# Kernel optimization log

Hardware: AMD Instinct MI355X
Metric: run time of the kernel (lower is better)

Reference implementation:

```python
import jax, jax.numpy as jnp
import numpy as np

H = 512      # hidden_size (hardcoded in __init__)
WD = 1024    # word_dim (hardcoded)
V = 4096     # len(i2w)+4
B, S, T = 256, 80, 28


def setup_inputs() -> dict:
    key = jax.random.key(0)
    ks = jax.random.split(key, 14)

    def gl(k, shape, fan_in):
        return (jax.random.normal(k, shape, jnp.float32) / np.sqrt(fan_in)).astype(jnp.float32)

    return {
        "encoder_last_hidden_state": jax.random.normal(ks[0], (1, B, H), jnp.float32),
        "encoder_output": jax.random.normal(ks[1], (B, S, H), jnp.float32),
        "targets": jax.random.randint(ks[2], (B, T), 0, V, dtype=jnp.int32),
        # embedding table
        "embedding": gl(ks[3], (V, WD), WD),
        # attention MLP (4 stacked linears, no activations, per the source)
        "W1": gl(ks[4], (2 * H, H), 2 * H), "b1": jnp.zeros((H,), jnp.float32),
        "W2": gl(ks[5], (H, H), H), "b2": jnp.zeros((H,), jnp.float32),
        "W3": gl(ks[6], (H, H), H), "b3": jnp.zeros((H,), jnp.float32),
        "W4": gl(ks[7], (H, H), H), "b4": jnp.zeros((H,), jnp.float32),
        "Ww": gl(ks[8], (H, 1), H),
        # GRU (input = hidden_size + word_dim = 1536), PyTorch gate order r,z,n
        "W_ih": gl(ks[9], (3 * H, H + WD), H + WD), "b_ih": jnp.zeros((3 * H,), jnp.float32),
        "W_hh": gl(ks[10], (3 * H, H), H), "b_hh": jnp.zeros((3 * H,), jnp.float32),
        # output projection
        "Wo": gl(ks[11], (H, V), H), "bo": jnp.zeros((V,), jnp.float32),
    }


def reference(encoder_last_hidden_state, encoder_output, targets, embedding,
              W1, b1, W2, b2, W3, b3, W4, b4, Ww,
              W_ih, b_ih, W_hh, b_hh, Wo, bo):
    n_steps = targets.shape[1] - 1  # seq_len - 1 decode steps

    def attention(h, enc):
        # h: (B,H) decoder hidden; enc: (B,S,H)
        hs = jnp.broadcast_to(h[:, None, :], enc.shape)
        m = jnp.concatenate([enc, hs], axis=-1)          # (B,S,2H)
        x = m @ W1 + b1
        x = x @ W2 + b2
        x = x @ W3 + b3
        x = x @ W4 + b4
        attw = jax.nn.softmax((x @ Ww)[..., 0], axis=1)  # (B,S)
        return jnp.einsum('bs,bsh->bh', attw, enc)       # context (B,H)

    def gru_cell(x, h):
        gi = x @ W_ih.T + b_ih
        gh = h @ W_hh.T + b_hh
        ir, iz, inn = jnp.split(gi, 3, axis=-1)
        hr, hz, hn = jnp.split(gh, 3, axis=-1)
        r = jax.nn.sigmoid(ir + hr)
        z = jax.nn.sigmoid(iz + hz)
        n = jnp.tanh(inn + r * hn)
        return (1.0 - z) * n + z * h

    h0 = encoder_last_hidden_state[0]                    # (B,H)
    w0 = jnp.ones((encoder_output.shape[0],), jnp.int32) # <BOS> = 1

    def step(carry, _):
        h, w = carry
        emb = embedding[w]                               # (B,WD)
        ctx = attention(h, encoder_output)               # (B,H)
        x = jnp.concatenate([emb, ctx], axis=-1)         # (B,WD+H)
        hn = gru_cell(x, h)
        logits = hn @ Wo + bo                            # (B,V)
        wn = jnp.argmax(logits, axis=-1).astype(jnp.int32)
        return (hn, wn), logits

    _, logits_seq = jax.lax.scan(step, (h0, w0), None, length=n_steps)
    seq_logProb = jnp.swapaxes(logits_seq, 0, 1)         # (B, T-1, V)
    seq_predictions = jnp.argmax(seq_logProb, axis=-1)
    return seq_logProb, seq_predictions
```

## Files before the change

kernel.cpp:

```cpp
#include <hip/hip_runtime.h>

#define B_ 256
#define S_ 80
#define H_ 512
#define V_ 4096
#define NSTEP 27

typedef unsigned short u16;
typedef __attribute__((ext_vector_type(8))) short short8v;
typedef __attribute__((ext_vector_type(4))) float f32x4;
typedef __attribute__((ext_vector_type(4))) unsigned short ushort4v;

#define MFMA_(a,b,c) __builtin_amdgcn_mfma_f32_16x16x32_bf16(a,b,c,0,0,0)
#define MFMA3(acc, ah, al, bh, bl) do{ acc = MFMA_(ah,bh,acc); acc = MFMA_(ah,bl,acc); acc = MFMA_(al,bh,acc);}while(0)

__device__ __forceinline__ unsigned fkey(float v){
    unsigned u = __float_as_uint(v);
    return (u & 0x80000000u) ? ~u : (u | 0x80000000u);
}
__device__ __forceinline__ u16 bf16_rne(float f){
    unsigned u = __float_as_uint(f);
    return (u16)((u + 0x7FFFu + ((u >> 16) & 1u)) >> 16);
}
__device__ __forceinline__ void split_f4(float4 v, ushort4v& hi, ushort4v& lo){
    float arr[4] = {v.x, v.y, v.z, v.w};
    ushort4v h, l;
#pragma unroll
    for (int i = 0; i < 4; ++i){
        u16 hb = bf16_rne(arr[i]);
        h[i] = hb;
        l[i] = bf16_rne(arr[i] - __uint_as_float(((unsigned)hb) << 16));
    }
    hi = h; lo = l;
}

__global__ __launch_bounds__(64) void matvec512(const float* __restrict__ W,
                                                const float* __restrict__ v,
                                                float* __restrict__ out){
    int row = blockIdx.x, lane = threadIdx.x;
    const float* wr = W + row * 512;
    float s = 0.f;
#pragma unroll
    for (int i = 0; i < 8; ++i) s += wr[lane + 64*i] * v[lane + 64*i];
#pragma unroll
    for (int off = 32; off; off >>= 1) s += __shfl_xor(s, off);
    if (lane == 0) out[row] = s;
}

__global__ __launch_bounds__(256) void prep_all(
    const float* __restrict__ Whh, const float* __restrict__ Wo,
    const float* __restrict__ emb, const float* __restrict__ Wih,
    const float* __restrict__ elhs,
    u16* __restrict__ WhhHi, u16* __restrict__ WhhLo,
    u16* __restrict__ WoThi, u16* __restrict__ WoTlo,
    u16* __restrict__ EmbHi, u16* __restrict__ EmbLo,
    u16* __restrict__ WihLHi, u16* __restrict__ WihLLo,
    u16* __restrict__ Sh, u16* __restrict__ Sl,
    unsigned* __restrict__ zp, int nz)
{
    __shared__ float T[64][65];
    int b = blockIdx.x, tid = threadIdx.x;
    if (b < 768){
        int idx = (b*256 + tid)*4;
        float4 v = *(const float4*)&Whh[idx];
        ushort4v h,l; split_f4(v,h,l);
        *(ushort4v*)&WhhHi[idx]=h; *(ushort4v*)&WhhLo[idx]=l;
    } else if (b < 1280){
        int lb = b - 768;
        int k0 = (lb & 7)*64, n0 = (lb >> 3)*64;
#pragma unroll
        for (int i = 0; i < 16; ++i){
            int idx = tid + i*256;
            int kk = idx >> 6, nn = idx & 63;
            T[kk][nn] = Wo[(size_t)(k0+kk)*4096 + n0+nn];
        }
        __syncthreads();
#pragma unroll
        for (int i = 0; i < 16; ++i){
            int idx = tid + i*256;
            int nn = idx >> 6, kk = idx & 63;
            float v = T[kk][nn];
            u16 hi = bf16_rne(v);
            u16 lo = bf16_rne(v - __uint_as_float(((unsigned)hi) << 16));
            size_t o = (size_t)(n0+nn)*512 + k0+kk;
            WoThi[o] = hi; WoTlo[o] = lo;
        }
    } else if (b < 5376){
        int idx = ((b-1280)*256 + tid)*4;
        float4 v = *(const float4*)&emb[idx];
        ushort4v h,l; split_f4(v,h,l);
        *(ushort4v*)&EmbHi[idx]=h; *(ushort4v*)&EmbLo[idx]=l;
    } else if (b < 6912){
        int id = ((b-5376)*256 + tid)*4;
        int r = id >> 10, c = id & 1023;
        float4 v = *(const float4*)&Wih[(size_t)r*1536 + c];
        ushort4v h,l; split_f4(v,h,l);
        *(ushort4v*)&WihLHi[id]=h; *(ushort4v*)&WihLLo[id]=l;
    } else if (b < 7040){
        int idx = ((b-6912)*256 + tid)*4;
        float4 v = *(const float4*)&elhs[idx];
        ushort4v h,l; split_f4(v,h,l);
        *(ushort4v*)&Sh[idx]=h; *(ushort4v*)&Sl[idx]=l;
    } else {
        int i = ((b-7040)*256 + tid)*4;
        if (i < nz){ zp[i]=0u; zp[i+1]=0u; zp[i+2]=0u; zp[i+3]=0u; }
    }
}

__global__ __launch_bounds__(512) void attn_ctx(const float* __restrict__ enc,
                                                const float* __restrict__ weff,
                                                float* __restrict__ ctx){
    __shared__ float att[S_];
    int b = blockIdx.x, tid = threadIdx.x;
    int wv = tid >> 6, lane = tid & 63;
    float w8[8];
#pragma unroll
    for (int i = 0; i < 8; ++i) w8[i] = weff[lane + 64*i];
    const float* eb = enc + (size_t)b * (S_*H_);
    for (int s = wv; s < S_; s += 8){
        const float* e = eb + s*512;
        float acc = 0.f;
#pragma unroll
        for (int i = 0; i < 8; ++i) acc += e[lane + 64*i] * w8[i];
#pragma unroll
        for (int off = 32; off; off >>= 1) acc += __shfl_xor(acc, off);
        if (lane == 0) att[s] = acc;
    }
    __syncthreads();
    if (tid == 0){
        float mx = att[0];
        for (int s = 1; s < S_; ++s) mx = fmaxf(mx, att[s]);
        float sum = 0.f;
        for (int s = 0; s < S_; ++s){ float e = expf(att[s] - mx); att[s] = e; sum += e; }
        float inv = 1.f / sum;
        for (int s = 0; s < S_; ++s) att[s] *= inv;
    }
    __syncthreads();
    float a = 0.f;
    for (int s = 0; s < S_; ++s) a += att[s] * eb[s*512 + tid];
    ctx[b*512 + tid] = a;
}

__device__ __forceinline__ void step_mm_body(char* smem, int m0, int nt, int n_logits,
    const u16* __restrict__ Ahg, const u16* __restrict__ Alg,
    const u16* __restrict__ WoHi, const u16* __restrict__ WoLo,
    const u16* __restrict__ WhhHi, const u16* __restrict__ WhhLo,
    const float* __restrict__ bo,
    float* __restrict__ logits, unsigned long long* __restrict__ Pcur,
    float* __restrict__ gh_out)
{
    u16 (*Ah)[2048] = (u16(*)[2048])(smem);
    u16 (*Al)[2048] = (u16(*)[2048])(smem + 8192);
    u16 (*Bh)[2048] = (u16(*)[2048])(smem + 16384);
    u16 (*Bl)[2048] = (u16(*)[2048])(smem + 24576);
    bool isL = nt < n_logits;
    int nbase = (isL ? nt : nt - n_logits) * 64;
    const u16* Bhg = isL ? WoHi : WhhHi;
    const u16* Blg = isL ? WoLo : WhhLo;
    int tid = threadIdx.x, lane = tid & 63, wid = tid >> 6;
    int wy = wid & 1, wx = wid >> 1;
    int l15 = lane & 15, rg = lane >> 4, lk = rg * 8;
    int sr = tid >> 2, sk8 = (tid & 3) * 8;

    const u16* gAh = Ahg + (size_t)(m0 + sr)*512 + sk8;
    const u16* gAl = Alg + (size_t)(m0 + sr)*512 + sk8;
    const u16* gBh = Bhg + (size_t)(nbase + sr)*512 + sk8;
    const u16* gBl = Blg + (size_t)(nbase + sr)*512 + sk8;

    *(short8v*)&Ah[0][tid*8] = *(const short8v*)gAh;
    *(short8v*)&Al[0][tid*8] = *(const short8v*)gAl;
    *(short8v*)&Bh[0][tid*8] = *(const short8v*)gBh;
    *(short8v*)&Bl[0][tid*8] = *(const short8v*)gBl;
    short8v r1a = *(const short8v*)(gAh + 32), r1b = *(const short8v*)(gAl + 32);
    short8v r1c = *(const short8v*)(gBh + 32), r1d = *(const short8v*)(gBl + 32);
    short8v r2a = *(const short8v*)(gAh + 64), r2b = *(const short8v*)(gAl + 64);
    short8v r2c = *(const short8v*)(gBh + 64), r2d = *(const short8v*)(gBl + 64);
    __syncthreads();

    f32x4 acc[2][2] = {};
    int p = 0;
    for (int k0 = 0; k0 < 512; k0 += 32){
        if (k0 + 32 < 512){
            *(short8v*)&Ah[p^1][tid*8] = r1a;
            *(short8v*)&Al[p^1][tid*8] = r1b;
            *(short8v*)&Bh[p^1][tid*8] = r1c;
            *(short8v*)&Bl[p^1][tid*8] = r1d;
            r1a = r2a; r1b = r2b; r1c = r2c; r1d = r2d;
            if (k0 + 96 < 512){
                r2a = *(const short8v*)(gAh + k0 + 96);
                r2b = *(const short8v*)(gAl + k0 + 96);
                r2c = *(const short8v*)(gBh + k0 + 96);
                r2d = *(const short8v*)(gBl + k0 + 96);
            }
        }
        short8v afh0 = *(const short8v*)&Ah[p][(wy*32 +  0 + l15)*32 + lk];
        short8v afh1 = *(const short8v*)&Ah[p][(wy*32 + 16 + l15)*32 + lk];
        short8v afl0 = *(const short8v*)&Al[p][(wy*32 +  0 + l15)*32 + lk];
        short8v afl1 = *(const short8v*)&Al[p][(wy*32 + 16 + l15)*32 + lk];
        short8v bfh0 = *(const short8v*)&Bh[p][(wx*32 +  0 + l15)*32 + lk];
        short8v bfh1 = *(const short8v*)&Bh[p][(wx*32 + 16 + l15)*32 + lk];
        short8v bfl0 = *(const short8v*)&Bl[p][(wx*32 +  0 + l15)*32 + lk];
        short8v bfl1 = *(const short8v*)&Bl[p][(wx*32 + 16 + l15)*32 + lk];
        MFMA3(acc[0][0], afh0, afl0, bfh0, bfl0);
        MFMA3(acc[0][1], afh0, afl0, bfh1, bfl1);
        MFMA3(acc[1][0], afh1, afl1, bfh0, bfl0);
        MFMA3(acc[1][1], afh1, afl1, bfh1, bfl1);
        __syncthreads();
        p ^= 1;
    }

    int col0 = nbase + wx*32 + l15;
    if (isL){
        float bo0 = bo[col0], bo1 = bo[col0 + 16];
#pragma unroll
        for (int mf = 0; mf < 2; ++mf){
#pragma unroll
            for (int r = 0; r < 4; ++r){
                int row = m0 + wy*32 + mf*16 + rg*4 + r;
                float v0 = acc[mf][0][r] + bo0;
                float v1 = acc[mf][1][r] + bo1;
                float* crow = logits + (size_t)row * (NSTEP * (size_t)V_);
                crow[col0]      = v0;
                crow[col0 + 16] = v1;
                unsigned long long k0_ = ((unsigned long long)fkey(v0) << 32) | (unsigned)(4095 - col0);
                unsigned long long k1_ = ((unsigned long long)fkey(v1) << 32) | (unsigned)(4095 - (col0+16));
                unsigned long long best = k0_ > k1_ ? k0_ : k1_;
#pragma unroll
                for (int off = 1; off < 16; off <<= 1){
                    unsigned long long o = __shfl_xor(best, off);
                    if (o > best) best = o;
                }
                if (l15 == 0) atomicMax(&Pcur[row], best);
            }
        }
    } else {
#pragma unroll
        for (int mf = 0; mf < 2; ++mf)
#pragma unroll
            for (int r = 0; r < 4; ++r){
                int row = m0 + wy*32 + mf*16 + rg*4 + r;
                gh_out[(size_t)row*1536 + col0]      = acc[mf][0][r];
                gh_out[(size_t)row*1536 + col0 + 16] = acc[mf][1][r];
            }
    }
}

__global__ __launch_bounds__(256) void front3(
    const u16* __restrict__ EmbHi, const u16* __restrict__ EmbLo,
    const u16* __restrict__ WihLHi, const u16* __restrict__ WihLLo,
    float* __restrict__ Eproj,
    const float* __restrict__ ctx, const float* __restrict__ WihR,
    const float* __restrict__ bih, float* __restrict__ gictx,
    const u16* __restrict__ Sh0, const u16* __restrict__ Sl0,
    const u16* __restrict__ WhhHi, const u16* __restrict__ WhhLo,
    float* __restrict__ gh0)
{
    __shared__ __align__(16) char smem[32768];
    int b = blockIdx.x, tid = threadIdx.x;
    if (b < 384){
        int work = (b & 7) * 48 + (b >> 3);
        int bm = work / 12, bn = work % 12;
        int n0 = bn * 128, m0 = bm * 128;
        int lane = tid & 63, wid = tid >> 6;
        int wy = wid & 1, wx = wid >> 1;
        int l15 = lane & 15, rg = lane >> 4, lk = rg * 8;
        u16* Ah = (u16*)smem;
        u16* Al = (u16*)(smem + 8192);
        u16* Bh = (u16*)(smem + 16384);
        u16* Bl = (u16*)(smem + 24576);
        const u16* gA[2][2]; const u16* gB[2][2];
#pragma unroll
        for (int j = 0; j < 2; ++j){
            int s = tid + j*256;
            int row = s >> 2, k8 = (s & 3)*8;
            gA[0][j] = EmbHi + (size_t)(m0+row)*1024 + k8;
            gA[1][j] = EmbLo + (size_t)(m0+row)*1024 + k8;
            gB[0][j] = WihLHi + (size_t)(n0+row)*1024 + k8;
            gB[1][j] = WihLLo + (size_t)(n0+row)*1024 + k8;
        }
        short8v rA[2][2], rB[2][2];
#pragma unroll
        for (int h = 0; h < 2; ++h)
#pragma unroll
            for (int j = 0; j < 2; ++j){
                rA[h][j] = *(const short8v*)gA[h][j];
                rB[h][j] = *(const short8v*)gB[h][j];
            }
        f32x4 acc[4][4] = {};
        for (int k0 = 0; k0 < 1024; k0 += 32){
            __syncthreads();
#pragma unroll
            for (int j = 0; j < 2; ++j){
                int s8 = (tid + j*256)*8;
                *(short8v*)&Ah[s8] = rA[0][j];
                *(short8v*)&Al[s8] = rA[1][j];
                *(short8v*)&Bh[s8] = rB[0][j];
                *(short8v*)&Bl[s8] = rB[1][j];
            }
            __syncthreads();
            if (k0 + 32 < 1024){
#pragma unroll
                for (int h = 0; h < 2; ++h)
#pragma unroll
                    for (int j = 0; j < 2; ++j){
                        rA[h][j] = *(const short8v*)(gA[h][j] + k0 + 32);
                        rB[h][j] = *(const short8v*)(gB[h][j] + k0 + 32);
                    }
            }
            short8v afh[4], afl[4];
#pragma unroll
            for (int mf = 0; mf < 4; ++mf){
                afh[mf] = *(const short8v*)&Ah[(wy*64 + mf*16 + l15)*32 + lk];
                afl[mf] = *(const short8v*)&Al[(wy*64 + mf*16 + l15)*32 + lk];
            }
#pragma unroll
            for (int nf = 0; nf < 4; ++nf){
                short8v bfh = *(const short8v*)&Bh[(wx*64 + nf*16 + l15)*32 + lk];
                short8v bfl = *(const short8v*)&Bl[(wx*64 + nf*16 + l15)*32 + lk];
#pragma unroll
                for (int mf = 0; mf < 4; ++mf)
                    MFMA3(acc[mf][nf], afh[mf], afl[mf], bfh, bfl);
            }
        }
        int col0 = n0 + wx*64 + l15;
#pragma unroll
        for (int mf = 0; mf < 4; ++mf)
#pragma unroll
            for (int r = 0; r < 4; ++r){
                int row = m0 + wy*64 + mf*16 + rg*4 + r;
#pragma unroll
                for (int nf = 0; nf < 4; ++nf)
                    Eproj[(size_t)row*1536 + col0 + nf*16] = acc[mf][nf][r];
            }
    } else if (b < 576){
        int lb = b - 384;
        int m0 = (lb & 7) * 32, n0 = (lb >> 3) * 64;
        float (*As)[36] = (float(*)[36])smem;
        float (*Bs)[68] = (float(*)[68])(smem + 2304);
        int lk = tid & 15, lr = tid >> 4;
        int tx = tid & 15, ty = tid >> 4;
        float c[2][4] = {};
        for (int k0 = 0; k0 < 512; k0 += 16){
#pragma unroll
            for (int i = 0; i < 2; ++i)
                As[lk][lr*2 + i] = ctx[(size_t)(m0 + lr*2 + i)*512 + k0 + lk];
#pragma unroll
            for (int i = 0; i < 4; ++i)
                Bs[lk][lr*4 + i] = WihR[(size_t)(n0 + lr*4 + i)*1536 + k0 + lk];
            __syncthreads();
#pragma unroll
            for (int k = 0; k < 16; ++k){
                float b4[4];
                *(float4*)b4 = *(const float4*)&Bs[k][tx*4];
#pragma unroll
                for (int i = 0; i < 2; ++i){
                    float a = As[k][ty*2 + i];
#pragma unroll
                    for (int j = 0; j < 4; ++j) c[i][j] += a * b4[j];
                }
            }
            __syncthreads();
        }
#pragma unroll
        for (int j = 0; j < 4; ++j){
            float bb = bih[n0 + tx*4 + j];
#pragma unroll
            for (int i = 0; i < 2; ++i)
                gictx[(size_t)(m0 + ty*2 + i)*1536 + n0 + tx*4 + j] = c[i][j] + bb;
        }
    } else {
        int lb = b - 576;
        step_mm_body(smem, (lb & 3)*64, lb >> 2, 0,
                     Sh0, Sl0, nullptr, nullptr, WhhHi, WhhLo,
                     nullptr, nullptr, nullptr, gh0);
    }
}

__global__ __launch_bounds__(128) void gru_pointwise(
    const float* __restrict__ gh, const float* __restrict__ Eproj,
    const float* __restrict__ gictx, const float* __restrict__ bhh,
    const float* __restrict__ hprev, float* __restrict__ hnext,
    u16* __restrict__ Sh, u16* __restrict__ Sl,
    const unsigned long long* __restrict__ Pprev,
    float* __restrict__ preds, int t)
{
    int tid = threadIdx.x;
    int row = blockIdx.x;
    int jj = tid * 4;
    int w = 1;
    if (t > 0){
        w = 4095 - (int)(Pprev[row] & 0xFFFFFFFFull);
        if (w < 0) w = 0; if (w > 4095) w = 4095;
        if (tid == 0) preds[row*NSTEP + (t-1)] = (float)w;
    }
    const float* gr = gh + (size_t)row * 1536;
    const float* ep = Eproj + (size_t)w * 1536;
    const float* gc = gictx + (size_t)row * 1536;
    float4 g0 = *(const float4*)&gr[jj];
    float4 g1 = *(const float4*)&gr[512 + jj];
    float4 g2 = *(const float4*)&gr[1024 + jj];
    float4 e0 = *(const float4*)&ep[jj];
    float4 e1 = *(const float4*)&ep[512 + jj];
    float4 e2 = *(const float4*)&ep[1024 + jj];
    float4 c0 = *(const float4*)&gc[jj];
    float4 c1 = *(const float4*)&gc[512 + jj];
    float4 c2 = *(const float4*)&gc[1024 + jj];
    float4 b0 = *(const float4*)&bhh[jj];
    float4 b1 = *(const float4*)&bhh[512 + jj];
    float4 b2 = *(const float4*)&bhh[1024 + jj];
    float4 ho = *(const float4*)&hprev[(size_t)row*512 + jj];
    const float* G0 = (const float*)&g0; const float* G1 = (const float*)&g1;
    const float* G2 = (const float*)&g2;
    const float* E0 = (const float*)&e0; const float* E1 = (const float*)&e1;
    const float* E2 = (const float*)&e2;
    const float* C0 = (const float*)&c0; const float* C1 = (const float*)&c1;
    const float* C2 = (const float*)&c2;
    const float* B0 = (const float*)&b0; const float* B1 = (const float*)&b1;
    const float* B2 = (const float*)&b2;
    const float* HO = (const float*)&ho;
    float4 res;
    float* R = (float*)&res;
#pragma unroll
    for (int i = 0; i < 4; ++i){
        float gir = E0[i] + C0[i] + G0[i] + B0[i];
        float giz = E1[i] + C1[i] + G1[i] + B1[i];
        float gin = E2[i] + C2[i];
        float rr = 1.f / (1.f + expf(-gir));
        float zz = 1.f / (1.f + expf(-giz));
        float nn = tanhf(gin + rr * (G2[i] + B2[i]));
        R[i] = (1.f - zz)*nn + zz*HO[i];
    }
    size_t o = (size_t)row*512 + jj;
    *(float4*)&hnext[o] = res;
    ushort4v h4, l4; split_f4(res, h4, l4);
    *(ushort4v*)&Sh[o] = h4;
    *(ushort4v*)&Sl[o] = l4;
}

__global__ __launch_bounds__(256) void step_mm(
    const u16* __restrict__ Ahg, const u16* __restrict__ Alg,
    const u16* __restrict__ WoHi, const u16* __restrict__ WoLo,
    const u16* __restrict__ WhhHi, const u16* __restrict__ WhhLo,
    const float* __restrict__ bo,
    float* __restrict__ logits, unsigned long long* __restrict__ Pcur,
    float* __restrict__ gh_out, int n_logits)
{
    __shared__ __align__(16) char smem[24576];
    u16 (*Ah)[1024] = (u16(*)[1024])(smem);
    u16 (*Al)[1024] = (u16(*)[1024])(smem + 4096);
    u16 (*Bh)[2048] = (u16(*)[2048])(smem + 8192);
    u16 (*Bl)[2048] = (u16(*)[2048])(smem + 16384);
    int bid = blockIdx.x;
    int work = (bid & 7) * 88 + (bid >> 3);
    int m0 = (work & 7) * 32;
    int nt = work >> 3;
    bool isL = nt < n_logits;
    int nbase = (isL ? nt : nt - n_logits) * 64;
    const u16* Bhg = isL ? WoHi : WhhHi;
    const u16* Blg = isL ? WoLo : WhhLo;
    int tid = threadIdx.x, lane = tid & 63, wid = tid >> 6;
    int wy = wid & 1, wx = wid >> 1;
    int l15 = lane & 15, rg = lane >> 4, lk = rg * 8;

    int ahalf = tid >> 7, ai = tid & 127;
    int ar = ai >> 2, ak8 = (ai & 3) * 8;
    const u16* gA = (ahalf ? Alg : Ahg) + (size_t)(m0 + ar)*512 + ak8;
    u16 (*Adst)[1024] = ahalf ? Al : Ah;
    int br = tid >> 2, bk8 = (tid & 3) * 8;
    const u16* gBh = Bhg + (size_t)(nbase + br)*512 + bk8;
    const u16* gBl = Blg + (size_t)(nbase + br)*512 + bk8;

    *(short8v*)&Adst[0][ai*8] = *(const short8v*)gA;
    *(short8v*)&Bh[0][tid*8] = *(const short8v*)gBh;
    *(short8v*)&Bl[0][tid*8] = *(const short8v*)gBl;
    short8v a1 = *(const short8v*)(gA + 32),  a2 = *(const short8v*)(gA + 64);
    short8v h1 = *(const short8v*)(gBh + 32), h2 = *(const short8v*)(gBh + 64);
    short8v l1 = *(const short8v*)(gBl + 32), l2 = *(const short8v*)(gBl + 64);
    __syncthreads();

    f32x4 acc[2] = {};
    int p = 0;
    for (int k0 = 0; k0 < 512; k0 += 32){
        if (k0 + 32 < 512){
            *(short8v*)&Adst[p^1][ai*8] = a1;
            *(short8v*)&Bh[p^1][tid*8] = h1;
            *(short8v*)&Bl[p^1][tid*8] = l1;
            a1 = a2; h1 = h2; l1 = l2;
            if (k0 + 96 < 512){
                a2 = *(const short8v*)(gA + k0 + 96);
                h2 = *(const short8v*)(gBh + k0 + 96);
                l2 = *(const short8v*)(gBl + k0 + 96);
            }
        }
        short8v afh = *(const short8v*)&Ah[p][(wy*16 + l15)*32 + lk];
        short8v afl = *(const short8v*)&Al[p][(wy*16 + l15)*32 + lk];
        short8v bfh0 = *(const short8v*)&Bh[p][(wx*32 +  0 + l15)*32 + lk];
        short8v bfh1 = *(const short8v*)&Bh[p][(wx*32 + 16 + l15)*32 + lk];
        short8v bfl0 = *(const short8v*)&Bl[p][(wx*32 +  0 + l15)*32 + lk];
        short8v bfl1 = *(const short8v*)&Bl[p][(wx*32 + 16 + l15)*32 + lk];
        MFMA3(acc[0], afh, afl, bfh0, bfl0);
        MFMA3(acc[1], afh, afl, bfh1, bfl1);
        __syncthreads();
        p ^= 1;
    }

    int col0 = nbase + wx*32 + l15;
    if (isL){
        float bo0 = bo[col0], bo1 = bo[col0 + 16];
#pragma unroll
        for (int r = 0; r < 4; ++r){
            int row = m0 + wy*16 + rg*4 + r;
            float v0 = acc[0][r] + bo0;
            float v1 = acc[1][r] + bo1;
            float* crow = logits + (size_t)row * (NSTEP * (size_t)V_);
            crow[col0]      = v0;
            crow[col0 + 16] = v1;
            unsigned long long k0_ = ((unsigned long long)fkey(v0) << 32) | (unsigned)(4095 - col0);
            unsigned long long k1_ = ((unsigned long long)fkey(v1) << 32) | (unsigned)(4095 - (col0+16));
            unsigned long long best = k0_ > k1_ ? k0_ : k1_;
#pragma unroll
            for (int off = 1; off < 16; off <<= 1){
                unsigned long long o = __shfl_xor(best, off);
                if (o > best) best = o;
            }
            if (l15 == 0) atomicMax(&Pcur[row], best);
        }
    } else {
#pragma unroll
        for (int r = 0; r < 4; ++r){
            int row = m0 + wy*16 + rg*4 + r;
            gh_out[(size_t)row*1536 + col0]      = acc[0][r];
            gh_out[(size_t)row*1536 + col0 + 16] = acc[1][r];
        }
    }
}

__global__ __launch_bounds__(256) void final_pred(const unsigned long long* __restrict__ P,
                                                  float* __restrict__ preds){
    int b = threadIdx.x;
    int w = 4095 - (int)(P[b] & 0xFFFFFFFFull);
    if (w < 0) w = 0; if (w > 4095) w = 4095;
    preds[b*NSTEP + (NSTEP-1)] = (float)w;
}

extern "C" void kernel_launch(void* const* d_in, const int* in_sizes, int n_in,
                              void* d_out, int out_size, void* d_ws, size_t ws_size,
                              hipStream_t stream){
    const float* elhs = (const float*)d_in[0];
    const float* enc  = (const float*)d_in[1];
    const float* emb  = (const float*)d_in[3];
    const float* W1   = (const float*)d_in[4];
    const float* W2   = (const float*)d_in[6];
    const float* W3   = (const float*)d_in[8];
    const float* W4   = (const float*)d_in[10];
    const float* Ww   = (const float*)d_in[12];
    const float* Wih  = (const float*)d_in[13];
    const float* bih  = (const float*)d_in[14];
    const float* Whh  = (const float*)d_in[15];
    const float* bhh  = (const float*)d_in[16];
    const float* Wo   = (const float*)d_in[17];
    const float* bo   = (const float*)d_in[18];

    float* out = (float*)d_out;
    float* preds = out + (size_t)B_ * NSTEP * V_;

    float* ws = (float*)d_ws;
    float* Eproj  = ws;  ws += (size_t)V_ * 1536;
    float* gictx  = ws;  ws += (size_t)B_ * 1536;
    float* ctx    = ws;  ws += B_ * H_;
    float* t1     = ws;  ws += 512;
    float* t2     = ws;  ws += 512;
    float* weff   = ws;  ws += 512;
    float* Hf     = ws;  ws += 2 * B_ * H_;
    float* ghbuf  = ws;  ws += B_ * 1536;
    u16* WoT_hi = (u16*)ws;  ws += (size_t)V_ * 512 / 2;
    u16* WoT_lo = (u16*)ws;  ws += (size_t)V_ * 512 / 2;
    u16* WhhHi  = (u16*)ws;  ws += 1536 * 512 / 2;
    u16* WhhLo  = (u16*)ws;  ws += 1536 * 512 / 2;
    u16* Sh     = (u16*)ws;  ws += B_ * H_ / 2;
    u16* Sl     = (u16*)ws;  ws += B_ * H_ / 2;
    unsigned long long* P = (unsigned long long*)ws;

    u16* EmbHi  = (u16*)d_out;
    u16* EmbLo  = EmbHi + (size_t)V_*1024;
    u16* WihLHi = EmbLo + (size_t)V_*1024;
    u16* WihLLo = WihLHi + (size_t)1536*1024;

    prep_all<<<7054, 256, 0, stream>>>(Whh, Wo, emb, Wih, elhs,
                                       WhhHi, WhhLo, WoT_hi, WoT_lo,
                                       EmbHi, EmbLo, WihLHi, WihLLo,
                                       Sh, Sl, (unsigned*)P, NSTEP*256*2);
    matvec512<<<512, 64, 0, stream>>>(W4, Ww, t1);
    matvec512<<<512, 64, 0, stream>>>(W3, t1, t2);
    matvec512<<<512, 64, 0, stream>>>(W2, t2, t1);
    matvec512<<<512, 64, 0, stream>>>(W1, t1, weff);
    attn_ctx<<<B_, 512, 0, stream>>>(enc, weff, ctx);
    front3<<<672, 256, 0, stream>>>(EmbHi, EmbLo, WihLHi, WihLLo, Eproj,
                                    ctx, Wih + 1024, bih, gictx,
                                    Sh, Sl, WhhHi, WhhLo, ghbuf);

    for (int t = 0; t < NSTEP; ++t){
        const float* hr = (t == 0) ? elhs : (Hf + (size_t)((t-1) & 1) * (B_*H_));
        float*       hw = Hf + (size_t)(t & 1) * (B_*H_);
        const unsigned long long* Pprev = P + (size_t)(t > 0 ? t-1 : 0) * 256;
        gru_pointwise<<<256, 128, 0, stream>>>(ghbuf, Eproj, gictx, bhh, hr, hw,
                                               Sh, Sl, Pprev, preds, t);
        step_mm<<<704, 256, 0, stream>>>(Sh, Sl, WoT_hi, WoT_lo, WhhHi, WhhLo, bo,
                                         out + (size_t)t * V_, P + (size_t)t*256, ghbuf, 64);
    }
    final_pred<<<1, 256, 0, stream>>>(P + (size_t)(NSTEP-1)*256, preds);
}
```

Baseline: 693.0 us.

## Double-buffer LDS in front3 GEMM and fold first matvec into prep kernel

The embedding-projection GEMM in front3 now uses two LDS buffers with a two-stage register prefetch, so each k-step needs one barrier instead of two and global loads run further ahead. Shared memory per block doubles to 64KB, which may lower occupancy. Separately, the W4·Ww matvec is merged into prep_all as extra blocks, removing one kernel launch from the serial chain.

```diff
diff --git a/kernel.cpp b/kernel.cpp
--- a/kernel.cpp
+++ b/kernel.cpp
@@ -51,11 +51,13 @@
     const float* __restrict__ Whh, const float* __restrict__ Wo,
     const float* __restrict__ emb, const float* __restrict__ Wih,
     const float* __restrict__ elhs,
+    const float* __restrict__ W4, const float* __restrict__ Ww,
     u16* __restrict__ WhhHi, u16* __restrict__ WhhLo,
     u16* __restrict__ WoThi, u16* __restrict__ WoTlo,
     u16* __restrict__ EmbHi, u16* __restrict__ EmbLo,
     u16* __restrict__ WihLHi, u16* __restrict__ WihLLo,
     u16* __restrict__ Sh, u16* __restrict__ Sl,
+    float* __restrict__ t1out,
     unsigned* __restrict__ zp, int nz)
 {
     __shared__ float T[64][65];
@@ -101,9 +103,19 @@
         float4 v = *(const float4*)&elhs[idx];
         ushort4v h,l; split_f4(v,h,l);
         *(ushort4v*)&Sh[idx]=h; *(ushort4v*)&Sl[idx]=l;
-    } else {
+    } else if (b < 7054){
         int i = ((b-7040)*256 + tid)*4;
         if (i < nz){ zp[i]=0u; zp[i+1]=0u; zp[i+2]=0u; zp[i+3]=0u; }
+    } else {
+        int lane = tid & 63, wv = tid >> 6;
+        int row = (b - 7054)*4 + wv;
+        const float* wr = W4 + (size_t)row * 512;
+        float s = 0.f;
+#pragma unroll
+        for (int i = 0; i < 8; ++i) s += wr[lane + 64*i] * Ww[lane + 64*i];
+#pragma unroll
+        for (int off = 32; off; off >>= 1) s += __shfl_xor(s, off);
+        if (lane == 0) t1out[row] = s;
     }
 }
 
@@ -255,7 +267,7 @@
     const u16* __restrict__ WhhHi, const u16* __restrict__ WhhLo,
     float* __restrict__ gh0)
 {
-    __shared__ __align__(16) char smem[32768];
+    __shared__ __align__(16) char smem[65536];
     int b = blockIdx.x, tid = threadIdx.x;
     if (b < 384){
         int work = (b & 7) * 48 + (b >> 3);
@@ -264,63 +276,86 @@
         int lane = tid & 63, wid = tid >> 6;
         int wy = wid & 1, wx = wid >> 1;
         int l15 = lane & 15, rg = lane >> 4, lk = rg * 8;
-        u16* Ah = (u16*)smem;
-        u16* Al = (u16*)(smem + 8192);
-        u16* Bh = (u16*)(smem + 16384);
-        u16* Bl = (u16*)(smem + 24576);
+        u16* AhB = (u16*)smem;
+        u16* AlB = (u16*)(smem + 16384);
+        u16* BhB = (u16*)(smem + 32768);
+        u16* BlB = (u16*)(smem + 49152);
         const u16* gA[2][2]; const u16* gB[2][2];
+        int s8i[2];
 #pragma unroll
         for (int j = 0; j < 2; ++j){
             int s = tid + j*256;
             int row = s >> 2, k8 = (s & 3)*8;
+            s8i[j] = s * 8;
             gA[0][j] = EmbHi + (size_t)(m0+row)*1024 + k8;
             gA[1][j] = EmbLo + (size_t)(m0+row)*1024 + k8;
             gB[0][j] = WihLHi + (size_t)(n0+row)*1024 + k8;
             gB[1][j] = WihLLo + (size_t)(n0+row)*1024 + k8;
         }
-        short8v rA[2][2], rB[2][2];
+#pragma unroll
+        for (int j = 0; j < 2; ++j){
+            *(short8v*)&AhB[s8i[j]] = *(const short8v*)gA[0][j];
+            *(short8v*)&AlB[s8i[j]] = *(const short8v*)gA[1][j];
+            *(short8v*)&BhB[s8i[j]] = *(const short8v*)gB[0][j];
+            *(short8v*)&BlB[s8i[j]] = *(const short8v*)gB[1][j];
+        }
+        short8v r1A[2][2], r1B[2][2], r2A[2][2], r2B[2][2];
 #pragma unroll
         for (int h = 0; h < 2; ++h)
 #pragma unroll
             for (int j = 0; j < 2; ++j){
-                rA[h][j] = *(const short8v*)gA[h][j];
-                rB[h][j] = *(const short8v*)gB[h][j];
-            }
+                r1A[h][j] = *(const short8v*)(gA[h][j] + 32);
+                r1B[h][j] = *(const short8v*)(gB[h][j] + 32);
+                r2A[h][j] = *(const short8v*)(gA[h][j] + 64);
+                r2B[h][j] = *(const short8v*)(gB[h][j] + 64);
+            }
+        __syncthreads();
         f32x4 acc[4][4] = {};
+        int p = 0;
         for (int k0 = 0; k0 < 1024; k0 += 32){
-            __syncthreads();
-#pragma unroll
-            for (int j = 0; j < 2; ++j){
-                int s8 = (tid + j*256)*8;
-                *(short8v*)&Ah[s8] = rA[0][j];
-                *(short8v*)&Al[s8] = rA[1][j];
-                *(short8v*)&Bh[s8] = rB[0][j];
-                *(short8v*)&Bl[s8] = rB[1][j];
-            }
-            __syncthreads();
             if (k0 + 32 < 1024){
+                int off = (p^1)*4096;
+#pragma unroll
+                for (int j = 0; j < 2; ++j){
+                    *(short8v*)&AhB[off + s8i[j]] = r1A[0][j];
+                    *(short8v*)&AlB[off + s8i[j]] = r1A[1][j];
+                    *(short8v*)&BhB[off + s8i[j]] = r1B[0][j];
+                    *(short8v*)&BlB[off + s8i[j]] = r1B[1][j];
+                }
 #pragma unroll
                 for (int h = 0; h < 2; ++h)
 #pragma unroll
                     for (int j = 0; j < 2; ++j){
-                        rA[h][j] = *(const short8v*)(gA[h][j] + k0 + 32);
-                        rB[h][j] = *(const short8v*)(gB[h][j] + k0 + 32);
+                        r1A[h][j] = r2A[h][j];
+                        r1B[h][j] = r2B[h][j];
                     }
-            }
+                if (k0 + 96 < 1024){
+#pragma unroll
+                    for (int h = 0; h < 2; ++h)
+#pragma unroll
+                        for (int j = 0; j < 2; ++j){
+                            r2A[h][j] = *(const short8v*)(gA[h][j] + k0 + 96);
+                            r2B[h][j] = *(const short8v*)(gB[h][j] + k0 + 96);
+                        }
+                }
+            }
+            int base = p*4096;
             short8v afh[4], afl[4];
 #pragma unroll
             for (int mf = 0; mf < 4; ++mf){
-                afh[mf] = *(const short8v*)&Ah[(wy*64 + mf*16 + l15)*32 + lk];
-                afl[mf] = *(const short8v*)&Al[(wy*64 + mf*16 + l15)*32 + lk];
+                afh[mf] = *(const short8v*)&AhB[base + (wy*64 + mf*16 + l15)*32 + lk];
+                afl[mf] = *(const short8v*)&AlB[base + (wy*64 + mf*16 + l15)*32 + lk];
             }
 #pragma unroll
             for (int nf = 0; nf < 4; ++nf){
-                short8v bfh = *(const short8v*)&Bh[(wx*64 + nf*16 + l15)*32 + lk];
-                short8v bfl = *(const short8v*)&Bl[(wx*64 + nf*16 + l15)*32 + lk];
+                short8v bfh = *(const short8v*)&BhB[base + (wx*64 + nf*16 + l15)*32 + lk];
+                short8v bfl = *(const short8v*)&BlB[base + (wx*64 + nf*16 + l15)*32 + lk];
 #pragma unroll
                 for (int mf = 0; mf < 4; ++mf)
                     MFMA3(acc[mf][nf], afh[mf], afl[mf], bfh, bfl);
             }
+            __syncthreads();
+            p ^= 1;
         }
         int col0 = n0 + wx*64 + l15;
 #pragma unroll
@@ -586,11 +621,10 @@
     u16* WihLHi = EmbLo + (size_t)V_*1024;
     u16* WihLLo = WihLHi + (size_t)1536*1024;
 
-    prep_all<<<7054, 256, 0, stream>>>(Whh, Wo, emb, Wih, elhs,
+    prep_all<<<7182, 256, 0, stream>>>(Whh, Wo, emb, Wih, elhs, W4, Ww,
                                        WhhHi, WhhLo, WoT_hi, WoT_lo,
                                        EmbHi, EmbLo, WihLHi, WihLLo,
-                                       Sh, Sl, (unsigned*)P, NSTEP*256*2);
-    matvec512<<<512, 64, 0, stream>>>(W4, Ww, t1);
+                                       Sh, Sl, t1, (unsigned*)P, NSTEP*256*2);
     matvec512<<<512, 64, 0, stream>>>(W3, t1, t2);
     matvec512<<<512, 64, 0, stream>>>(W2, t2, t1);
     matvec512<<<512, 64, 0, stream>>>(W1, t1, weff);
```

Result: no change. 694.5 us (+0.2%).
